# Kernel optimization log

Hardware: AMD Instinct MI355X
Metric: run time of the kernel (lower is better)

## Reference

```python
import jax, jax.numpy as jnp
import numpy as np

IN_F = 3072       # in_features
OUT_F = 9216      # out_features = 3 * N_HEADS * HEAD_DIM (fused QKV)
GROUP = 64        # quantization group size
RANK = 32         # lora_rank
HEAD_DIM = 128
N_HEADS = OUT_F // (3 * HEAD_DIM)  # 24
EPS = 1e-6
LORA_SCALE = 1.0


def setup_inputs() -> dict:
    key = jax.random.key(0)
    ks = jax.random.split(key, 10)
    B, S = 1, 4096
    x = jax.random.normal(ks[0], (B, S, IN_F), dtype=jnp.float32)
    # packed int4 weights: two signed int4 values per int8 byte
    qweight = jax.random.randint(ks[1], (OUT_F, IN_F // 2), -128, 128, dtype=jnp.int32).astype(jnp.int8)
    wscales = (jax.random.uniform(ks[2], (IN_F // GROUP, OUT_F)) * 0.02 + 0.001).astype(jnp.float32)
    bias = (jax.random.normal(ks[3], (OUT_F,)) * 0.01).astype(jnp.float32)
    lora_down = (jax.random.normal(ks[4], (IN_F, RANK)) * 0.02).astype(jnp.float32)
    lora_up = (jax.random.normal(ks[5], (OUT_F, RANK)) * 0.02).astype(jnp.float32)
    smooth = (jax.random.uniform(ks[6], (IN_F,)) * 0.5 + 0.75).astype(jnp.float32)   # keep away from 0
    norm_q = (jax.random.uniform(ks[7], (HEAD_DIM,)) * 0.5 + 0.75).astype(jnp.float32)
    norm_k = (jax.random.uniform(ks[8], (HEAD_DIM,)) * 0.5 + 0.75).astype(jnp.float32)
    ang = jax.random.uniform(ks[9], (S, HEAD_DIM // 2)) * (2.0 * np.pi)
    rotary_emb = jnp.stack([jnp.cos(ang), jnp.sin(ang)], axis=-1).astype(jnp.float32)  # [S, D/2, 2]
    return dict(x=x, qweight=qweight, wscales=wscales, bias=bias, lora_down=lora_down,
                lora_up=lora_up, smooth=smooth, norm_q=norm_q, norm_k=norm_k, rotary_emb=rotary_emb)


def _dequant_weight(qweight, wscales):
    # unpack two signed int4 lanes from each int8 (low nibble first), then per-group scale
    low = jnp.right_shift(jnp.left_shift(qweight, 4), 4)   # arithmetic shifts on int8 -> sign extend
    high = jnp.right_shift(qweight, 4)
    w4 = jnp.stack([low, high], axis=-1).reshape(OUT_F, IN_F)          # int4 codes in [-8, 7]
    wg = w4.astype(jnp.float32).reshape(OUT_F, IN_F // GROUP, GROUP)
    return (wg * wscales.T[:, :, None]).reshape(OUT_F, IN_F)          # [N, K]


def _quantize_act(x, smooth, lora_down):
    # fused: smooth -> symmetric per-token per-group int4 quantize -> lora_down projection
    B, S, K = x.shape
    M = B * S
    xs = (x / smooth).reshape(M, K)
    xg = xs.reshape(M, K // GROUP, GROUP)
    ascale = jnp.max(jnp.abs(xg), axis=-1, keepdims=True) / 7.0
    ascale = jnp.maximum(ascale, 1e-8)
    q = jnp.clip(jnp.round(xg / ascale), -8.0, 7.0)
    deq = (q * ascale).reshape(M, K)                                   # dequantized int4 activation
    lora_act = xs @ lora_down                                          # [M, RANK], fp32 side path
    return deq, lora_act


def _rope(t, cos, sin):
    # interleaved pairs (even, odd) rotation; t: [M, H, D], cos/sin: [M, 1, D/2]
    e, o = t[..., 0::2], t[..., 1::2]
    re = e * cos - o * sin
    ro = e * sin + o * cos
    return jnp.stack([re, ro], axis=-1).reshape(t.shape)


def reference(x, qweight, wscales, bias, lora_down, lora_up, smooth, norm_q, norm_k, rotary_emb):
    B, S, K = x.shape
    M = B * S
    deq_x, lora_act = _quantize_act(x, smooth, lora_down)
    w = _dequant_weight(qweight, wscales)
    # main int4 GEMM + LoRA up + bias, all fused in the real kernel
    out = deq_x @ w.T + (LORA_SCALE * lora_act) @ lora_up.T + bias     # [M, OUT_F]
    qkv = out.reshape(M, 3, N_HEADS, HEAD_DIM)
    q, k, v = qkv[:, 0], qkv[:, 1], qkv[:, 2]
    def rms(t, g):
        return t * jax.lax.rsqrt(jnp.mean(t * t, axis=-1, keepdims=True) + EPS) * g
    q = rms(q, norm_q)
    k = rms(k, norm_k)
    cos = rotary_emb[:, None, :, 0]   # [M, 1, D/2]
    sin = rotary_emb[:, None, :, 1]
    q = _rope(q, cos, sin)
    k = _rope(k, cos, sin)
    return jnp.stack([q, k, v], axis=1).reshape(B, S, OUT_F)
```

## Files before the change

### kernel.cpp

```cpp
#include <hip/hip_runtime.h>
#include <cstdint>

#define MDIM 4096
#define NDIM 9216
#define KDIM 3072
#define KP   3136
#define NKT  49

typedef unsigned int u32;
typedef unsigned short u16;
typedef float f32x4 __attribute__((ext_vector_type(4)));
typedef __bf16 bf16x8 __attribute__((ext_vector_type(8)));

__device__ __forceinline__ u16 f2bf(float f) {
  u32 u = __float_as_uint(f);
  u32 r = u + 0x7fffu + ((u >> 16) & 1u);
  return (u16)(r >> 16);
}

__device__ __forceinline__ float frcp(float f) { return __builtin_amdgcn_rcpf(f); }

__device__ __forceinline__ void gld_lds16(const void* g, void* l) {
  __builtin_amdgcn_global_load_lds((__attribute__((address_space(1))) void*)g,
                                   (__attribute__((address_space(3))) void*)l,
                                   16, 0, 0);
}

__global__ __launch_bounds__(256) void k_quant(const float* __restrict__ x, const float* __restrict__ smooth,
                        const float* __restrict__ lora_down, u16* __restrict__ Aex) {
  __shared__ float xs_s[KDIM];
  __shared__ float part[8][32];
  const int m = blockIdx.x;
  const int tid = threadIdx.x;
  const int sub = tid & 15;
  const float* xr = x + (size_t)m * KDIM;
  u16* arow = Aex + (size_t)m * KP;

  #pragma unroll
  for (int p = 0; p < 3; ++p) {
    int g = p * 16 + (tid >> 4);
    int k0 = g * 64 + sub * 4;
    float4 xv = *(const float4*)(xr + k0);
    float4 sv = *(const float4*)(smooth + k0);
    float a0 = xv.x * frcp(sv.x), a1 = xv.y * frcp(sv.y);
    float a2 = xv.z * frcp(sv.z), a3 = xv.w * frcp(sv.w);
    xs_s[k0+0] = a0; xs_s[k0+1] = a1; xs_s[k0+2] = a2; xs_s[k0+3] = a3;
    float am = fmaxf(fmaxf(fabsf(a0), fabsf(a1)), fmaxf(fabsf(a2), fabsf(a3)));
    am = fmaxf(am, __shfl_xor(am, 8, 16));
    am = fmaxf(am, __shfl_xor(am, 4, 16));
    am = fmaxf(am, __shfl_xor(am, 2, 16));
    am = fmaxf(am, __shfl_xor(am, 1, 16));
    float asc = fmaxf(am * (1.0f / 7.0f), 1e-8f);
    float iasc = frcp(asc);
    float q0 = fminf(7.f, fmaxf(-8.f, rintf(a0 * iasc)));
    float q1 = fminf(7.f, fmaxf(-8.f, rintf(a1 * iasc)));
    float q2 = fminf(7.f, fmaxf(-8.f, rintf(a2 * iasc)));
    float q3 = fminf(7.f, fmaxf(-8.f, rintf(a3 * iasc)));
    float d0 = q0 * asc, d1 = q1 * asc, d2 = q2 * asc, d3 = q3 * asc;
    u32 lo = (u32)f2bf(d0) | ((u32)f2bf(d1) << 16);
    u32 hi = (u32)f2bf(d2) | ((u32)f2bf(d3) << 16);
    *(uint2*)(arow + k0) = make_uint2(lo, hi);
  }
  if (tid < 32) arow[3104 + tid] = 0;
  __syncthreads();
  {
    int chunk = tid >> 5, r = tid & 31;
    float s = 0.f;
    int kb = chunk * 384;
    #pragma unroll 8
    for (int i = 0; i < 384; ++i)
      s += xs_s[kb + i] * lora_down[(size_t)(kb + i) * 32 + r];
    part[chunk][r] = s;
  }
  __syncthreads();
  if (tid < 32) {
    float s = 0.f;
    #pragma unroll
    for (int c = 0; c < 8; ++c) s += part[c][tid];
    arow[3072 + tid] = f2bf(s);
  }
}

#define DQ_BLOCKS 13824
__global__ __launch_bounds__(256) void k_wdq(const u32* __restrict__ qw, const float* __restrict__ wsc,
                      const float* __restrict__ lora_up, u16* __restrict__ Bex) {
  const int tid = threadIdx.x;
  if (blockIdx.x >= DQ_BLOCKS) {
    int idx = (blockIdx.x - DQ_BLOCKS) * 256 + tid;
    int n = idx >> 6, c = idx & 63;
    u16 v = 0;
    if (c < 32) v = f2bf(lora_up[n * 32 + c]);
    Bex[(size_t)n * KP + 3072 + c] = v;
    return;
  }
  __shared__ int s_viol;
  u32 probe = qw[tid];
  bool ok = (probe >> 8) == ((probe & 0x80u) ? 0xffffffu : 0u);
  if (tid == 0) s_viol = 0;
  __syncthreads();
  if (!ok) atomicOr(&s_viol, 1);
  __syncthreads();
  const int f = (s_viol == 0);

  int idx = blockIdx.x * 256 + tid;
  int n = idx / 384;
  int j = idx - n * 384;
  int k0 = j * 8;
  u32 w;
  if (f) {
    uint4 q4 = ((const uint4*)qw)[idx];
    w  = (q4.x & 0xffu) | ((q4.y & 0xffu) << 8) | ((q4.z & 0xffu) << 16) | ((q4.w & 0xffu) << 24);
  } else {
    w = qw[idx];
  }
  float ws = wsc[(k0 >> 6) * NDIM + n];
  u32 ow[4];
  #pragma unroll
  for (int b = 0; b < 4; ++b) {
    int by = (int)((w >> (8 * b)) & 0xffu);
    int lo = (by << 28) >> 28;
    int hi = (by << 24) >> 28;
    ow[b] = (u32)f2bf((float)lo * ws) | ((u32)f2bf((float)hi * ws) << 16);
  }
  *(uint4*)(Bex + (size_t)n * KP + k0) = make_uint4(ow[0], ow[1], ow[2], ow[3]);
}

__global__ __launch_bounds__(256) void k_gemm(const u16* __restrict__ A, const u16* __restrict__ B,
                                              const float* __restrict__ bias, const float* __restrict__ norm_q,
                                              const float* __restrict__ norm_k, const float* __restrict__ rot,
                                              float* __restrict__ out) {
  __shared__ __align__(16) u16 sA[128 * 64];
  __shared__ __align__(16) u16 sB[128 * 64];
  const int tid  = threadIdx.x;
  const int lane = tid & 63;
  const int wave = tid >> 6;
  const int m0 = blockIdx.y * 128;
  const int n0 = blockIdx.x * 128;
  const int wm = (wave >> 1) * 64;
  const int wn = (wave & 1) * 64;
  const int lr = lane & 15;
  const int lq = lane >> 4;

  f32x4 acc[4][4] = {};

  const u16* ga[4]; const u16* gb[4]; u16* la[4]; u16* lb[4];
  #pragma unroll
  for (int i = 0; i < 4; ++i) {
    int p = i * 256 + tid;
    int r = p >> 3;
    int c = (p & 7) ^ (r & 7);
    ga[i] = A + (size_t)(m0 + r) * KP + c * 8;
    gb[i] = B + (size_t)(n0 + r) * KP + c * 8;
    la[i] = &sA[p * 8];
    lb[i] = &sB[p * 8];
  }
  int aoff[2][4], boff[2][4];
  #pragma unroll
  for (int ks = 0; ks < 2; ++ks) {
    int cch = lq + ks * 4;
    #pragma unroll
    for (int t = 0; t < 4; ++t) {
      int rowa = wm + t * 16 + lr;
      int rowb = wn + t * 16 + lr;
      aoff[ks][t] = rowa * 64 + ((cch ^ (rowa & 7)) * 8);
      boff[ks][t] = rowb * 64 + ((cch ^ (rowb & 7)) * 8);
    }
  }

  for (int kt = 0; kt < NKT; ++kt) {
    #pragma unroll
    for (int i = 0; i < 4; ++i) { gld_lds16(ga[i], la[i]); ga[i] += 64; }
    #pragma unroll
    for (int i = 0; i < 4; ++i) { gld_lds16(gb[i], lb[i]); gb[i] += 64; }
    asm volatile("s_waitcnt vmcnt(0)" ::: "memory");
    __syncthreads();
    #pragma unroll
    for (int ks = 0; ks < 2; ++ks) {
      bf16x8 af[4], bf[4];
      #pragma unroll
      for (int t = 0; t < 4; ++t) af[t] = *(const bf16x8*)&sA[aoff[ks][t]];
      #pragma unroll
      for (int t = 0; t < 4; ++t) bf[t] = *(const bf16x8*)&sB[boff[ks][t]];
      #pragma unroll
      for (int ti = 0; ti < 4; ++ti)
        #pragma unroll
        for (int tj = 0; tj < 4; ++tj)
          acc[ti][tj] = __builtin_amdgcn_mfma_f32_16x16x32_bf16(af[ti], bf[tj], acc[ti][tj], 0, 0, 0);
    }
    __syncthreads();
  }

  const int sel = (n0 >= 6144) ? 2 : ((n0 >= 3072) ? 1 : 0);

  #pragma unroll
  for (int tj = 0; tj < 4; ++tj) {
    float bv = bias[n0 + wn + tj * 16 + lr];
    #pragma unroll
    for (int ti = 0; ti < 4; ++ti)
      #pragma unroll
      for (int rg = 0; rg < 4; ++rg)
        acc[ti][tj][rg] += bv;
  }

  if (sel == 2) {
    #pragma unroll
    for (int tj = 0; tj < 4; ++tj) {
      int n = n0 + wn + tj * 16 + lr;
      #pragma unroll
      for (int ti = 0; ti < 4; ++ti) {
        int mrow = m0 + wm + ti * 16 + lq * 4;
        #pragma unroll
        for (int rg = 0; rg < 4; ++rg)
          out[(size_t)(mrow + rg) * NDIM + n] = acc[ti][tj][rg];
      }
    }
    return;
  }

  float part[4][4];
  #pragma unroll
  for (int ti = 0; ti < 4; ++ti)
    #pragma unroll
    for (int rg = 0; rg < 4; ++rg) {
      float s = 0.f;
      #pragma unroll
      for (int tj = 0; tj < 4; ++tj) s += acc[ti][tj][rg] * acc[ti][tj][rg];
      part[ti][rg] = s;
    }
  #pragma unroll
  for (int off = 1; off < 16; off <<= 1)
    #pragma unroll
    for (int ti = 0; ti < 4; ++ti)
      #pragma unroll
      for (int rg = 0; rg < 4; ++rg)
        part[ti][rg] += __shfl_xor(part[ti][rg], off);

  float* ssq = (float*)sA;
  #pragma unroll
  for (int ti = 0; ti < 4; ++ti)
    #pragma unroll
    for (int rg = 0; rg < 4; ++rg)
      if (lr == ti * 4 + rg)
        ssq[(wn >> 6) * 128 + wm + ti * 16 + lq * 4 + rg] = part[ti][rg];
  __syncthreads();

  const float* nrm = sel ? norm_k : norm_q;
  float gm[4];
  #pragma unroll
  for (int tj = 0; tj < 4; ++tj) gm[tj] = nrm[wn + tj * 16 + lr];
  const float2* rot2 = (const float2*)rot;
  const float sgn = (lr & 1) ? 1.0f : -1.0f;

  #pragma unroll
  for (int ti = 0; ti < 4; ++ti) {
    #pragma unroll
    for (int rg = 0; rg < 4; ++rg) {
      int row = wm + ti * 16 + lq * 4 + rg;
      float tot = ssq[row] + ssq[128 + row];
      float rs = rsqrtf(tot * (1.0f / 128.0f) + 1e-6f);
      int m = m0 + row;
      #pragma unroll
      for (int tj = 0; tj < 4; ++tj) {
        int nl = wn + tj * 16 + lr;
        float v = acc[ti][tj][rg] * rs * gm[tj];
        float p = __shfl_xor(v, 1);
        float2 cs = rot2[(size_t)m * 64 + (nl >> 1)];
        float r = v * cs.x + sgn * (p * cs.y);
        out[(size_t)m * NDIM + n0 + nl] = r;
      }
    }
  }
}

extern "C" void kernel_launch(void* const* d_in, const int* in_sizes, int n_in,
                              void* d_out, int out_size, void* d_ws, size_t ws_size,
                              hipStream_t stream) {
  const float* x         = (const float*)d_in[0];
  const u32*   qweight   = (const u32*)d_in[1];
  const float* wscales   = (const float*)d_in[2];
  const float* bias      = (const float*)d_in[3];
  const float* lora_down = (const float*)d_in[4];
  const float* lora_up   = (const float*)d_in[5];
  const float* smooth    = (const float*)d_in[6];
  const float* norm_q    = (const float*)d_in[7];
  const float* norm_k    = (const float*)d_in[8];
  const float* rot       = (const float*)d_in[9];
  float* out = (float*)d_out;

  u16* Aex = (u16*)d_ws;
  u16* Bex = Aex + (size_t)MDIM * KP;

  k_quant<<<MDIM, 256, 0, stream>>>(x, smooth, lora_down, Aex);
  k_wdq<<<DQ_BLOCKS + (NDIM * 64) / 256, 256, 0, stream>>>(qweight, wscales, lora_up, Bex);
  k_gemm<<<dim3(NDIM / 128, MDIM / 128), 256, 0, stream>>>(Aex, Bex, bias, norm_q, norm_k, rot, out);
}
```

Baseline: 608.8 us.

## Merge activation quant and weight dequant kernels, vectorize LoRA-down reduction

New measurement: 596.7 us. 1.02x faster.

```diff
diff --git a/kernel.cpp b/kernel.cpp
--- a/kernel.cpp
+++ b/kernel.cpp
@@ -7,6 +7,10 @@
 #define KP   3136
 #define NKT  49
 
+#define QB 4096
+#define WB 13824
+#define PB 2304
+
 typedef unsigned int u32;
 typedef unsigned short u16;
 typedef float f32x4 __attribute__((ext_vector_type(4)));
@@ -26,12 +30,59 @@
                                    16, 0, 0);
 }
 
-__global__ __launch_bounds__(256) void k_quant(const float* __restrict__ x, const float* __restrict__ smooth,
-                        const float* __restrict__ lora_down, u16* __restrict__ Aex) {
+__global__ __launch_bounds__(256) void k_prep(const float* __restrict__ x, const u32* __restrict__ qw,
+                        const float* __restrict__ wsc, const float* __restrict__ lora_down,
+                        const float* __restrict__ lora_up, const float* __restrict__ smooth,
+                        u16* __restrict__ Aex, u16* __restrict__ Bex) {
   __shared__ float xs_s[KDIM];
-  __shared__ float part[8][32];
-  const int m = blockIdx.x;
+  __shared__ float part[64 * 32];
   const int tid = threadIdx.x;
+  int bid = blockIdx.x;
+
+  if (bid >= QB) {
+    bid -= QB;
+    if (bid >= WB) {
+      int idx = (bid - WB) * 256 + tid;
+      int n = idx >> 6, c = idx & 63;
+      u16 v = 0;
+      if (c < 32) v = f2bf(lora_up[n * 32 + c]);
+      Bex[(size_t)n * KP + 3072 + c] = v;
+      return;
+    }
+    __shared__ int s_viol;
+    u32 probe = qw[tid];
+    bool ok = (probe >> 8) == ((probe & 0x80u) ? 0xffffffu : 0u);
+    if (tid == 0) s_viol = 0;
+    __syncthreads();
+    if (!ok) atomicOr(&s_viol, 1);
+    __syncthreads();
+    const int f = (s_viol == 0);
+
+    int idx = bid * 256 + tid;
+    int n = idx / 384;
+    int j = idx - n * 384;
+    int k0 = j * 8;
+    u32 w;
+    if (f) {
+      uint4 q4 = ((const uint4*)qw)[idx];
+      w = (q4.x & 0xffu) | ((q4.y & 0xffu) << 8) | ((q4.z & 0xffu) << 16) | ((q4.w & 0xffu) << 24);
+    } else {
+      w = qw[idx];
+    }
+    float ws = wsc[(k0 >> 6) * NDIM + n];
+    u32 ow[4];
+    #pragma unroll
+    for (int b = 0; b < 4; ++b) {
+      int by = (int)((w >> (8 * b)) & 0xffu);
+      int lo = (by << 28) >> 28;
+      int hi = (by << 24) >> 28;
+      ow[b] = (u32)f2bf((float)lo * ws) | ((u32)f2bf((float)hi * ws) << 16);
+    }
+    *(uint4*)(Bex + (size_t)n * KP + k0) = make_uint4(ow[0], ow[1], ow[2], ow[3]);
+    return;
+  }
+
+  const int m = bid;
   const int sub = tid & 15;
   const float* xr = x + (size_t)m * KDIM;
   u16* arow = Aex + (size_t)m * KP;
@@ -63,66 +114,34 @@
   }
   if (tid < 32) arow[3104 + tid] = 0;
   __syncthreads();
+
   {
-    int chunk = tid >> 5, r = tid & 31;
-    float s = 0.f;
-    int kb = chunk * 384;
-    #pragma unroll 8
-    for (int i = 0; i < 384; ++i)
-      s += xs_s[kb + i] * lora_down[(size_t)(kb + i) * 32 + r];
-    part[chunk][r] = s;
+    const int c  = tid >> 2;
+    const int r8 = (tid & 3) * 8;
+    float a[8] = {0.f, 0.f, 0.f, 0.f, 0.f, 0.f, 0.f, 0.f};
+    const float* lp = lora_down + (size_t)c * 32 + r8;
+    #pragma unroll 4
+    for (int i = 0; i < 48; ++i) {
+      float xv = xs_s[i * 64 + c];
+      float4 l0 = *(const float4*)(lp);
+      float4 l1 = *(const float4*)(lp + 4);
+      a[0] = fmaf(xv, l0.x, a[0]); a[1] = fmaf(xv, l0.y, a[1]);
+      a[2] = fmaf(xv, l0.z, a[2]); a[3] = fmaf(xv, l0.w, a[3]);
+      a[4] = fmaf(xv, l1.x, a[4]); a[5] = fmaf(xv, l1.y, a[5]);
+      a[6] = fmaf(xv, l1.z, a[6]); a[7] = fmaf(xv, l1.w, a[7]);
+      lp += 64 * 32;
+    }
+    __syncthreads();
+    *(float4*)(&part[c * 32 + r8])     = make_float4(a[0], a[1], a[2], a[3]);
+    *(float4*)(&part[c * 32 + r8 + 4]) = make_float4(a[4], a[5], a[6], a[7]);
   }
   __syncthreads();
   if (tid < 32) {
     float s = 0.f;
-    #pragma unroll
-    for (int c = 0; c < 8; ++c) s += part[c][tid];
+    #pragma unroll 8
+    for (int cc = 0; cc < 64; ++cc) s += part[cc * 32 + tid];
     arow[3072 + tid] = f2bf(s);
   }
-}
-
-#define DQ_BLOCKS 13824
-__global__ __launch_bounds__(256) void k_wdq(const u32* __restrict__ qw, const float* __restrict__ wsc,
-                      const float* __restrict__ lora_up, u16* __restrict__ Bex) {
-  const int tid = threadIdx.x;
-  if (blockIdx.x >= DQ_BLOCKS) {
-    int idx = (blockIdx.x - DQ_BLOCKS) * 256 + tid;
-    int n = idx >> 6, c = idx & 63;
-    u16 v = 0;
-    if (c < 32) v = f2bf(lora_up[n * 32 + c]);
-    Bex[(size_t)n * KP + 3072 + c] = v;
-    return;
-  }
-  __shared__ int s_viol;
-  u32 probe = qw[tid];
-  bool ok = (probe >> 8) == ((probe & 0x80u) ? 0xffffffu : 0u);
-  if (tid == 0) s_viol = 0;
-  __syncthreads();
-  if (!ok) atomicOr(&s_viol, 1);
-  __syncthreads();
-  const int f = (s_viol == 0);
-
-  int idx = blockIdx.x * 256 + tid;
-  int n = idx / 384;
-  int j = idx - n * 384;
-  int k0 = j * 8;
-  u32 w;
-  if (f) {
-    uint4 q4 = ((const uint4*)qw)[idx];
-    w  = (q4.x & 0xffu) | ((q4.y & 0xffu) << 8) | ((q4.z & 0xffu) << 16) | ((q4.w & 0xffu) << 24);
-  } else {
-    w = qw[idx];
-  }
-  float ws = wsc[(k0 >> 6) * NDIM + n];
-  u32 ow[4];
-  #pragma unroll
-  for (int b = 0; b < 4; ++b) {
-    int by = (int)((w >> (8 * b)) & 0xffu);
-    int lo = (by << 28) >> 28;
-    int hi = (by << 24) >> 28;
-    ow[b] = (u32)f2bf((float)lo * ws) | ((u32)f2bf((float)hi * ws) << 16);
-  }
-  *(uint4*)(Bex + (size_t)n * KP + k0) = make_uint4(ow[0], ow[1], ow[2], ow[3]);
 }
 
 __global__ __launch_bounds__(256) void k_gemm(const u16* __restrict__ A, const u16* __restrict__ B,
@@ -290,7 +309,6 @@
   u16* Aex = (u16*)d_ws;
   u16* Bex = Aex + (size_t)MDIM * KP;
 
-  k_quant<<<MDIM, 256, 0, stream>>>(x, smooth, lora_down, Aex);
-  k_wdq<<<DQ_BLOCKS + (NDIM * 64) / 256, 256, 0, stream>>>(qweight, wscales, lora_up, Bex);
+  k_prep<<<QB + WB + PB, 256, 0, stream>>>(x, qweight, wscales, lora_down, lora_up, smooth, Aex, Bex);
   k_gemm<<<dim3(NDIM / 128, MDIM / 128), 256, 0, stream>>>(Aex, Bex, bias, norm_q, norm_k, rot, out);
 }
```
